# Optimization experiments

Measured on AMD Instinct MI355X. Metric: run time of the kernel, lower is better.

Reference implementation:

```python
import jax, jax.numpy as jnp
import numpy as np

B, S, H = 4, 2048, 2048

def setup_inputs() -> dict:
    key = jax.random.key(0)
    k1, k2, k3 = jax.random.split(key, 3)
    xav_qkv = float(np.sqrt(6.0 / (H + 3 * H)))
    xav_out = float(np.sqrt(6.0 / (H + H)))
    return {
        "hidden_states": jax.random.normal(k1, (B, S, H), dtype=jnp.float32),
        "w_qkv": jax.random.uniform(k2, (3 * H, H), minval=-xav_qkv, maxval=xav_qkv, dtype=jnp.float32),
        "b_qkv": jnp.zeros((3 * H,), dtype=jnp.float32),
        "w_out": jax.random.uniform(k3, (H, H), minval=-xav_out, maxval=xav_out, dtype=jnp.float32),
        "b_out": jnp.zeros((H,), dtype=jnp.float32),
    }

def reference(hidden_states, w_qkv, b_qkv, w_out, b_out):
    Bc, Sc, Hc = hidden_states.shape
    scaling = jnp.sqrt(jnp.asarray(Hc, hidden_states.dtype))
    # qkv projection: torch Linear is x @ W^T + b
    qkv = jnp.einsum('bsh,oh->bso', hidden_states, w_qkv) + b_qkv  # [B,S,3H]
    q, k, v = jnp.split(qkv, 3, axis=-1)  # each [B,S,H]
    scores = jnp.einsum('bqh,bkh->bqk', q, k) / scaling  # [B,S,S]
    probs = jax.nn.softmax(scores, axis=-1)
    context = jnp.einsum('bqk,bkh->bqh', probs, v)  # [B,S,H]
    out = jnp.einsum('bsh,oh->bso', context, w_out) + b_out
    return out
```

## Files before the change

kernel.cpp:

```cpp
#include <hip/hip_runtime.h>
#include <cstdint>

typedef _Float16 f16;
typedef __attribute__((ext_vector_type(8))) _Float16 f16x8;
typedef __attribute__((ext_vector_type(4))) _Float16 f16x4;
typedef __attribute__((ext_vector_type(4))) float f32x4;

typedef __attribute__((address_space(1))) void gvoid_t;
typedef __attribute__((address_space(3))) void lvoid_t;

__device__ __forceinline__ void async_copy16(void* lds, const void* g) {
  __builtin_amdgcn_global_load_lds((gvoid_t*)(uintptr_t)g, (lvoid_t*)lds, 16, 0, 0);
}

#define BARRIER()   __builtin_amdgcn_s_barrier()
#define SCHEDBAR()  __builtin_amdgcn_sched_barrier(0)
#define VMCNT(n)    do { SCHEDBAR(); asm volatile("s_waitcnt vmcnt(" #n ")"); SCHEDBAR(); } while (0)

#define MFMA16(a, b, c) __builtin_amdgcn_mfma_f32_16x16x32_f16((a), (b), (c), 0, 0, 0)

template<int OUT_F16>
__device__ __forceinline__ void gemm_body(const f16* __restrict__ Ab, int lda,
                                          const f16* __restrict__ Bb, int ldb,
                                          void* __restrict__ Cz, int ldc,
                                          const float* __restrict__ bias,
                                          float scale, int K)
{
  __shared__ f16 AH0a[8192]; __shared__ f16 AH0b[8192];
  __shared__ f16 AH1a[8192]; __shared__ f16 AH1b[8192];
  __shared__ f16 BH0a[8192]; __shared__ f16 BH0b[8192];
  __shared__ f16 BH1a[8192]; __shared__ f16 BH1b[8192];

  const int tid = threadIdx.x, lane = tid & 63, wave = tid >> 6;
  const int wr = wave >> 2, wc = wave & 3;
  const int l15 = lane & 15, lk = lane >> 4;

  int lin = blockIdx.y * gridDim.x + blockIdx.x;
  const int nxy = gridDim.x * gridDim.y;
  if ((nxy & 7) == 0) lin = (lin & 7) * (nxy >> 3) + (lin >> 3);
  const int bx = lin % gridDim.x, by = lin / gridDim.x;

  const long brow = (long)by * 256, bcol = (long)bx * 256;

  const int r0  = tid >> 3;
  const int gc8 = (tid & 7) ^ (r0 & 7);
  const int sdst = wave * 512;

  const f16* gAa = Ab + (brow + r0) * (long)lda + gc8 * 8;
  const f16* gAb = gAa + 128L * lda;
  const f16* gBa = Bb + (bcol + r0) * (long)ldb + gc8 * 8;
  const f16* gBb = gBa + 128L * ldb;

#define STG(BUF, G, LD, KOFF) { \
    async_copy16(BUF + sdst,        (G) + (KOFF)); \
    async_copy16(BUF + 4096 + sdst, (G) + 64L * (LD) + (KOFF)); }

  const f16* myA0 = wr ? AH0b : AH0a;
  const f16* myA1 = wr ? AH1b : AH1a;
  const f16* myB0 = (wc & 2) ? BH0b : BH0a;
  const f16* myB1 = (wc & 2) ? BH1b : BH1a;

  const int x8   = l15 & 7;
  const int cb0  = (lk ^ x8) * 8;
  const int cb1  = ((4 | lk) ^ x8) * 8;
  const int lbA  = l15 * 64;
  const int lbB  = ((wc & 1) * 64 + l15) * 64;

#define RDA4(SRC, MP) { \
    af[0] = *(const f16x8*)&(SRC)[lbA + (2*(MP))   * 1024 + cb0]; \
    af[1] = *(const f16x8*)&(SRC)[lbA + (2*(MP))   * 1024 + cb1]; \
    af[2] = *(const f16x8*)&(SRC)[lbA + (2*(MP)+1) * 1024 + cb0]; \
    af[3] = *(const f16x8*)&(SRC)[lbA + (2*(MP)+1) * 1024 + cb1]; }

#define RDB8(SRC) { \
    bf[0][0] = *(const f16x8*)&(SRC)[lbB + 0 * 1024 + cb0]; \
    bf[1][0] = *(const f16x8*)&(SRC)[lbB + 0 * 1024 + cb1]; \
    bf[0][1] = *(const f16x8*)&(SRC)[lbB + 1 * 1024 + cb0]; \
    bf[1][1] = *(const f16x8*)&(SRC)[lbB + 1 * 1024 + cb1]; \
    bf[0][2] = *(const f16x8*)&(SRC)[lbB + 2 * 1024 + cb0]; \
    bf[1][2] = *(const f16x8*)&(SRC)[lbB + 2 * 1024 + cb1]; \
    bf[0][3] = *(const f16x8*)&(SRC)[lbB + 3 * 1024 + cb0]; \
    bf[1][3] = *(const f16x8*)&(SRC)[lbB + 3 * 1024 + cb1]; }

#define CLUSTER(MP) { \
    __builtin_amdgcn_s_setprio(1); \
    _Pragma("unroll") \
    for (int n = 0; n < 4; ++n) { \
      f32x4 t = MFMA16(af[0], bf[0][n], acc[2*(MP)][n]); \
      acc[2*(MP)][n] = MFMA16(af[1], bf[1][n], t); \
    } \
    _Pragma("unroll") \
    for (int n = 0; n < 4; ++n) { \
      f32x4 t = MFMA16(af[2], bf[0][n], acc[2*(MP)+1][n]); \
      acc[2*(MP)+1][n] = MFMA16(af[3], bf[1][n], t); \
    } \
    __builtin_amdgcn_s_setprio(0); }

  f32x4 acc[8][4] = {};
  f16x8 af[4], bf[2][4];
  const int NIT = K >> 7;

  STG(BH0a, gBa, ldb, 0);  STG(BH0b, gBb, ldb, 0);
  STG(AH0a, gAa, lda, 0);  STG(AH0b, gAb, lda, 0);
  STG(BH1a, gBa, ldb, 64);
  VMCNT(2);
  BARRIER();

  for (int J = 0; J < NIT; ++J) {
    const long k1 = 128L * J + 64;
    const long k2 = 128L * J + 128;
    const long k3 = 128L * J + 192;
    const bool st = (J + 1 < NIT);

    RDA4(myA0, 0); RDB8(myB0);
    STG(BH1b, gBb, ldb, k1);
    BARRIER(); CLUSTER(0);

    RDA4(myA0, 1);
    STG(AH1a, gAa, lda, k1);
    BARRIER(); CLUSTER(1);

    RDA4(myA0, 2);
    STG(AH1b, gAb, lda, k1);
    BARRIER(); CLUSTER(2);

    RDA4(myA0, 3);
    if (st) { STG(BH0a, gBa, ldb, k2); VMCNT(2); } else { VMCNT(0); }
    BARRIER(); CLUSTER(3);

    RDA4(myA1, 0); RDB8(myB1);
    if (st) STG(BH0b, gBb, ldb, k2);
    BARRIER(); CLUSTER(0);

    RDA4(myA1, 1);
    if (st) STG(AH0a, gAa, lda, k2);
    BARRIER(); CLUSTER(1);

    RDA4(myA1, 2);
    if (st) STG(AH0b, gAb, lda, k2);
    BARRIER(); CLUSTER(2);

    RDA4(myA1, 3);
    if (st) { STG(BH1a, gBa, ldb, k3); VMCNT(2); }
    BARRIER(); CLUSTER(3);
  }

#pragma unroll
  for (int m = 0; m < 8; ++m) {
#pragma unroll
    for (int n = 0; n < 4; ++n) {
      const long col = bcol + wc * 64 + n * 16 + l15;
      const float bv = bias ? bias[col] : 0.0f;
#pragma unroll
      for (int j = 0; j < 4; ++j) {
        const long row = brow + wr * 128 + m * 16 + lk * 4 + j;
        const float v = acc[m][n][j] * scale + bv;
        if (OUT_F16)
          ((f16*)Cz)[row * (long)ldc + col] = (f16)v;
        else
          ((float*)Cz)[row * (long)ldc + col] = v;
      }
    }
  }
#undef STG
#undef RDA4
#undef RDB8
#undef CLUSTER
}

template<int OUT_F16>
__global__ __launch_bounds__(512, 2)
void gemm256(const f16* __restrict__ A, int lda, long sA,
             const f16* __restrict__ B, int ldb, long sB,
             void* __restrict__ Cv, int ldc, long sC,
             const float* __restrict__ bias, float scale, int K)
{
  const int z = blockIdx.z;
  void* Cz = OUT_F16 ? (void*)((f16*)Cv + (long)z * sC)
                     : (void*)((float*)Cv + (long)z * sC);
  gemm_body<OUT_F16>(A + (long)z * sA, lda, B + (long)z * sB, ldb,
                     Cz, ldc, bias, scale, K);
}

__global__ __launch_bounds__(512, 2)
void gemm_sv(const f16* __restrict__ QKV, const f16* __restrict__ Wouth,
             f16* __restrict__ SCH, f16* __restrict__ VWT, float inv_sqrt_h)
{
  const int z = blockIdx.z;
  const long sQ = 2048L * 6144, sS = 2048L * 2048;
  if (z < 4) {
    gemm_body<1>(QKV + z * sQ, 6144, QKV + 2048 + z * sQ, 6144,
                 SCH + z * sS, 2048, nullptr, inv_sqrt_h, 2048);
  } else {
    const int zz = z - 4;
    gemm_body<1>(Wouth, 2048, QKV + 4096 + zz * sQ, 6144,
                 VWT + zz * sS, 2048, nullptr, 1.0f, 2048);
  }
}

__global__ void cast_all(const float* __restrict__ x,     f16* __restrict__ xh,
                         const float* __restrict__ wq,    f16* __restrict__ wqh,
                         const float* __restrict__ wo,    f16* __restrict__ woh)
{
  const int b = blockIdx.x;
  const float* in; f16* out; long n; int b0, nb;
  if (b < 2048)      { in = x;  out = xh;  n = 16777216L; b0 = 0;    nb = 2048; }
  else if (b < 3584) { in = wq; out = wqh; n = 12582912L; b0 = 2048; nb = 1536; }
  else               { in = wo; out = woh; n = 4194304L;  b0 = 3584; nb = 512;  }
  long i = ((long)(b - b0) * 256 + threadIdx.x) * 4;
  const long stride = (long)nb * 256 * 4;
  for (; i < n; i += stride) {
    const float4 v = *reinterpret_cast<const float4*>(in + i);
    f16x4 h;
    h.x = (f16)v.x; h.y = (f16)v.y; h.z = (f16)v.z; h.w = (f16)v.w;
    *reinterpret_cast<f16x4*>(out + i) = h;
  }
}

__global__ __launch_bounds__(256)
void softmax_rows(f16* __restrict__ scores) {
  const long row = blockIdx.x;
  f16* s = scores + row * 2048;
  const int tid = threadIdx.x;
  const int lane = tid & 63;
  const int wave = tid >> 6;

  const f16x8 hv = *reinterpret_cast<const f16x8*>(s + tid * 8);
  float v[8];
  float sum = 0.f;
#pragma unroll
  for (int j = 0; j < 8; ++j) { v[j] = __expf((float)hv[j]); sum += v[j]; }
#pragma unroll
  for (int off = 32; off >= 1; off >>= 1) sum += __shfl_xor(sum, off);
  __shared__ float red[4];
  if (lane == 0) red[wave] = sum;
  __syncthreads();
  const float inv = 1.0f / (red[0] + red[1] + red[2] + red[3]);

  f16x8 h;
#pragma unroll
  for (int j = 0; j < 8; ++j) h[j] = (f16)(v[j] * inv);
  *reinterpret_cast<f16x8*>(s + tid * 8) = h;
}

extern "C" void kernel_launch(void* const* d_in, const int* in_sizes, int n_in,
                              void* d_out, int out_size, void* d_ws, size_t ws_size,
                              hipStream_t stream) {
  const float* x     = (const float*)d_in[0];
  const float* w_qkv = (const float*)d_in[1];
  const float* b_qkv = (const float*)d_in[2];
  const float* w_out = (const float*)d_in[3];
  const float* b_out = (const float*)d_in[4];
  float* out = (float*)d_out;

  char* ws = (char*)d_ws;
  f16*   Xh    = (f16*)(ws + 0);
  f16*   Wqkvh = (f16*)(ws + 33554432L);
  f16*   Wouth = (f16*)(ws + 58720256L);
  f16*   QKV   = (f16*)(ws + 67108864L);
  f16*   SCH   = (f16*)(ws + 167772160L);
  f16*   VWT   = (f16*)(ws + 234881024L);

  const float inv_sqrt_h = 0.022097086912079608f;

  cast_all<<<4096, 256, 0, stream>>>(x, Xh, w_qkv, Wqkvh, w_out, Wouth);

  gemm256<1><<<dim3(24, 32, 1), 512, 0, stream>>>(
      Xh, 2048, 0, Wqkvh, 2048, 0, QKV, 6144, 0, b_qkv, 1.0f, 2048);

  gemm_sv<<<dim3(8, 8, 8), 512, 0, stream>>>(QKV, Wouth, SCH, VWT, inv_sqrt_h);

  softmax_rows<<<8192, 256, 0, stream>>>(SCH);

  gemm256<0><<<dim3(8, 8, 4), 512, 0, stream>>>(
      SCH, 2048, 2048L * 2048, VWT, 2048, 2048L * 2048,
      out, 2048, 2048L * 2048, b_out, 1.0f, 2048);
}
```

Baseline: 430.6 us.

## Halve barriers in GEMM main loop by grouping two MFMA clusters per barrier

Cuts the workgroup barriers in the pipelined GEMM inner loop from eight to four per iteration, so two MFMA clusters run between each barrier. The vmcnt wait moves after the cluster compute, and B fragment reads now come before A reads. The goal is to cut barrier stalls and let global-to-LDS copies overlap more compute. This risks a WAR/RAW race on the LDS half-buffers if a stage overwrite no longer lines up with the reads of other waves.

```diff
diff --git a/kernel.cpp b/kernel.cpp
--- a/kernel.cpp
+++ b/kernel.cpp
@@ -112,37 +112,39 @@
     const long k3 = 128L * J + 192;
     const bool st = (J + 1 < NIT);
 
-    RDA4(myA0, 0); RDB8(myB0);
+    RDB8(myB0); RDA4(myA0, 0);
     STG(BH1b, gBb, ldb, k1);
-    BARRIER(); CLUSTER(0);
-
+    CLUSTER(0);
     RDA4(myA0, 1);
     STG(AH1a, gAa, lda, k1);
-    BARRIER(); CLUSTER(1);
+    CLUSTER(1);
+    BARRIER();
 
     RDA4(myA0, 2);
     STG(AH1b, gAb, lda, k1);
-    BARRIER(); CLUSTER(2);
-
+    CLUSTER(2);
     RDA4(myA0, 3);
-    if (st) { STG(BH0a, gBa, ldb, k2); VMCNT(2); } else { VMCNT(0); }
-    BARRIER(); CLUSTER(3);
-
-    RDA4(myA1, 0); RDB8(myB1);
+    if (st) STG(BH0a, gBa, ldb, k2);
+    CLUSTER(3);
+    if (st) { VMCNT(2); } else { VMCNT(0); }
+    BARRIER();
+
+    RDB8(myB1); RDA4(myA1, 0);
     if (st) STG(BH0b, gBb, ldb, k2);
-    BARRIER(); CLUSTER(0);
-
+    CLUSTER(0);
     RDA4(myA1, 1);
     if (st) STG(AH0a, gAa, lda, k2);
-    BARRIER(); CLUSTER(1);
+    CLUSTER(1);
+    BARRIER();
 
     RDA4(myA1, 2);
     if (st) STG(AH0b, gAb, lda, k2);
-    BARRIER(); CLUSTER(2);
-
+    CLUSTER(2);
     RDA4(myA1, 3);
-    if (st) { STG(BH1a, gBa, ldb, k3); VMCNT(2); }
-    BARRIER(); CLUSTER(3);
+    if (st) STG(BH1a, gBa, ldb, k3);
+    CLUSTER(3);
+    if (st) VMCNT(2);
+    BARRIER();
   }
 
 #pragma unroll
```

Result: no change. 433.8 us (+0.8%).
